# Performance work log

Hardware: AMD Instinct MI355X
Metric: run time of the kernel (lower is better)

Reference implementation:

```python
import jax, jax.numpy as jnp
import numpy as np

TAU = 0.2
ALPHA = 0.8
EPS = 1e-8  # torch cosine_similarity eps
LAM_POS = 1.5  # generate_lambda()=0.5, +1 for extrapolation
LAM_NEG = 0.5  # interpolation lambda


def _cos_sim_matrix(x):
    # row-normalize with clamped norm (matches F.cosine_similarity eps), then gram matrix
    n = x / jnp.maximum(jnp.linalg.norm(x, axis=1, keepdims=True), EPS)
    return n @ n.T


def setup_inputs() -> dict:
    key = jax.random.key(0)
    N, D = 4096, 512
    emb = jax.random.normal(key, (N, D), dtype=jnp.float32)
    # SimCLR-style symmetric positive pairs: (2k,2k+1) and (2k+1,2k)
    base = np.arange(0, N, 2)
    fwd_pairs = np.stack([base, base + 1], axis=1)
    pairs = np.concatenate([fwd_pairs, fwd_pairs[:, ::-1]], axis=0)  # [N, 2]
    return {"embeddings": emb, "positive_pairs": jnp.asarray(pairs, dtype=jnp.int32)}


def reference(embeddings, positive_pairs):
    # stage == 'train' (quantile-thresholded hard-negative branch)
    N = embeddings.shape[0]
    ar = jnp.arange(N)
    pi, pj = positive_pairs[:, 0], positive_pairs[:, 1]
    # ordered positive mask (symmetric because pairs include both orientations)
    pos_mask = jnp.zeros((N, N), dtype=bool).at[pi, pj].set(True)

    # --- extrapolate positive pairs: row i -> 1.5*e_i - 0.5*e_j ---
    partner_pos = jnp.full((N,), -1, dtype=jnp.int32).at[pi].set(pj.astype(jnp.int32))
    in_pair = partner_pos >= 0
    pp = jnp.where(in_pair, partner_pos, 0)
    hard_pos_emb = jnp.where(
        in_pair[:, None],
        LAM_POS * embeddings - (LAM_POS - 1.0) * embeddings[pp],
        embeddings,
    )

    # --- interpolate negative pairs: row k -> 0.5*(e_k + e_partner) ---
    # Negative pairs are all ordered (i,j), i!=j, not positive, scattered in
    # row k is the largest i with (i,k) negative.
    valid = (~pos_mask.T) & (ar[None, :] != ar[:, None])  # valid[k, i] = (i,k) is negative
    partner_neg = jnp.max(jnp.where(valid, ar[None, :], -1), axis=1)
    hard_neg_emb = LAM_NEG * embeddings + (1.0 - LAM_NEG) * embeddings[partner_neg]

    # --- three NxN cosine-sim matrices, composed by the scatter pattern ---
    orig_sim = _cos_sim_matrix(embeddings)
    hard_pos_sim = _cos_sim_matrix(hard_pos_emb)
    hard_neg_sim = _cos_sim_matrix(hard_neg_emb)
    diag = jnp.eye(N, dtype=bool)
    sim = jnp.where(diag, orig_sim, jnp.where(pos_mask, hard_pos_sim, hard_neg_sim))

    # --- contrastive loss with per-row quantile hard-negative threshold ---
    mask = diag | pos_mask
    exp_sim = jnp.exp(sim / TAU)
    exp_masked = jnp.where(mask, 0.0, exp_sim)
    pos_sim = exp_sim[pi, pj]              # [P]
    exp_rows = exp_masked[pi]              # [P, N]
    thr = jnp.quantile(exp_rows, ALPHA, axis=1, keepdims=True)
    hard_neg_sum = jnp.sum(jnp.where(exp_rows >= thr, exp_rows, 0.0), axis=1)
    loss = -jnp.log(pos_sim / (pos_sim + hard_neg_sum))
    # torch sums loss_ij + loss_ji over all rows / (2*P); with symmetric pair
    # list this equals sum(loss_ij)/P
    return jnp.sum(loss) / positive_pairs.shape[0]
```

## Files before the change

kernel.cpp:

```cpp
#include <hip/hip_runtime.h>
#include <cmath>

#define DIM 512
#define TAU_INV 5.0f
#define EPSN 1e-8f
#define ALPHA_Q 0.8f
#define TPITCH 72

typedef __attribute__((ext_vector_type(8))) unsigned short us8;
typedef __attribute__((ext_vector_type(4))) unsigned short us4;
typedef __attribute__((ext_vector_type(8))) short s8v;
typedef __attribute__((ext_vector_type(4))) float f4;

__device__ __forceinline__ unsigned short f2h(float f) {
    _Float16 h = (_Float16)f;
    return *(const unsigned short*)&h;
}
__device__ __forceinline__ float h2f(unsigned u) {
    unsigned short us = (unsigned short)u;
    _Float16 h = *(const _Float16*)&us;
    return (float)h;
}
__device__ __forceinline__ unsigned key16(unsigned u) {
    return u ^ (0x8000u | (0x7FFFu & (0u - (u >> 15))));
}
__device__ __forceinline__ float keyval(unsigned k) {
    unsigned u = (k & 0x8000u) ? (k & 0x7FFFu) : ((~k) & 0xFFFFu);
    return h2f(u);
}

__global__ void k_scatter(const int* __restrict__ pairs, int* partner, int P) {
    int k = blockIdx.x * 256 + threadIdx.x;
    if (k < P) partner[pairs[2 * k]] = pairs[2 * k + 1];
}

__global__ __launch_bounds__(64) void k_prep(const float* __restrict__ emb,
                                             const int* __restrict__ partner,
                                             const int* __restrict__ pairs,
                                             unsigned short* __restrict__ mb,
                                             float* __restrict__ pos_term,
                                             int N, int P) {
    int bid = blockIdx.x, t = threadIdx.x;
    if (bid < N) {
        int i = bid;
        int q = N - 1;
        if (q == i || partner[q] == i) q = N - 2;
        if (q == i || partner[q] == i) q = N - 3;
        const float4* A = (const float4*)(emb + (size_t)i * DIM);
        const float4* B = (const float4*)(emb + (size_t)q * DIM);
        float4 a0 = A[t], a1 = A[t + 64];
        float4 b0 = B[t], b1 = B[t + 64];
        float h0x = 0.5f * (a0.x + b0.x), h0y = 0.5f * (a0.y + b0.y);
        float h0z = 0.5f * (a0.z + b0.z), h0w = 0.5f * (a0.w + b0.w);
        float h1x = 0.5f * (a1.x + b1.x), h1y = 0.5f * (a1.y + b1.y);
        float h1z = 0.5f * (a1.z + b1.z), h1w = 0.5f * (a1.w + b1.w);
        float ss = h0x * h0x + h0y * h0y + h0z * h0z + h0w * h0w
                 + h1x * h1x + h1y * h1y + h1z * h1z + h1w * h1w;
        for (int o = 32; o > 0; o >>= 1) ss += __shfl_xor(ss, o);
        float inv = 1.0f / fmaxf(sqrtf(ss), EPSN);
        us4 lo, hi;
        lo[0] = f2h(h0x * inv); lo[1] = f2h(h0y * inv);
        lo[2] = f2h(h0z * inv); lo[3] = f2h(h0w * inv);
        hi[0] = f2h(h1x * inv); hi[1] = f2h(h1y * inv);
        hi[2] = f2h(h1z * inv); hi[3] = f2h(h1w * inv);
        *(us4*)(mb + (size_t)i * DIM + t * 4) = lo;
        *(us4*)(mb + (size_t)i * DIM + 256 + t * 4) = hi;
    } else {
        int k = bid - N;
        int i = pairs[2 * k], j = pairs[2 * k + 1];
        const float4* A = (const float4*)(emb + (size_t)i * DIM);
        const float4* B = (const float4*)(emb + (size_t)j * DIM);
        float4 a0 = A[t], a1 = A[t + 64];
        float4 b0 = B[t], b1 = B[t + 64];
        float dab = 0.f, naa = 0.f, nbb = 0.f;
        float fa, fb;
        fa = 1.5f * a0.x - 0.5f * b0.x; fb = 1.5f * b0.x - 0.5f * a0.x; dab += fa * fb; naa += fa * fa; nbb += fb * fb;
        fa = 1.5f * a0.y - 0.5f * b0.y; fb = 1.5f * b0.y - 0.5f * a0.y; dab += fa * fb; naa += fa * fa; nbb += fb * fb;
        fa = 1.5f * a0.z - 0.5f * b0.z; fb = 1.5f * b0.z - 0.5f * a0.z; dab += fa * fb; naa += fa * fa; nbb += fb * fb;
        fa = 1.5f * a0.w - 0.5f * b0.w; fb = 1.5f * b0.w - 0.5f * a0.w; dab += fa * fb; naa += fa * fa; nbb += fb * fb;
        fa = 1.5f * a1.x - 0.5f * b1.x; fb = 1.5f * b1.x - 0.5f * a1.x; dab += fa * fb; naa += fa * fa; nbb += fb * fb;
        fa = 1.5f * a1.y - 0.5f * b1.y; fb = 1.5f * b1.y - 0.5f * a1.y; dab += fa * fb; naa += fa * fa; nbb += fb * fb;
        fa = 1.5f * a1.z - 0.5f * b1.z; fb = 1.5f * b1.z - 0.5f * a1.z; dab += fa * fb; naa += fa * fa; nbb += fb * fb;
        fa = 1.5f * a1.w - 0.5f * b1.w; fb = 1.5f * b1.w - 0.5f * a1.w; dab += fa * fb; naa += fa * fa; nbb += fb * fb;
        for (int o = 32; o > 0; o >>= 1) {
            dab += __shfl_xor(dab, o);
            naa += __shfl_xor(naa, o);
            nbb += __shfl_xor(nbb, o);
        }
        if (t == 0) {
            float sim = dab / (fmaxf(sqrtf(naa), EPSN) * fmaxf(sqrtf(nbb), EPSN));
            pos_term[k] = expf(sim * TAU_INV);
        }
    }
}

__global__ __launch_bounds__(256, 3) void k_gemm_sym(const unsigned short* __restrict__ mb,
                                                     unsigned short* __restrict__ S, int N) {
    __shared__ __align__(16) unsigned short smem[4 * 64 * TPITCH];
    int tid = threadIdx.x;
    int wave = tid >> 6, lane = tid & 63, quad = lane >> 4, l16 = lane & 15;
    int wr = (wave >> 1) * 64, wc = (wave & 1) * 64;

    int ntb = N >> 7;
    int bi = 0, rem = blockIdx.x, rowlen = ntb;
    while (rem >= rowlen) { rem -= rowlen; ++bi; --rowlen; }
    int bj = bi + rem;
    int iBase = bi * 128, jBase = bj * 128;
    int lrow = lane >> 2, lseg = lane & 3;

    const unsigned short* gA0 = mb + (size_t)(iBase + wave * 32 + lrow) * DIM + lseg * 8;
    const unsigned short* gA1 = gA0 + 16 * DIM;
    const unsigned short* gB0 = mb + (size_t)(jBase + wave * 32 + lrow) * DIM + lseg * 8;
    const unsigned short* gB1 = gB0 + 16 * DIM;

    __attribute__((address_space(3))) char* ldsBase =
        (__attribute__((address_space(3))) char*)smem;
    __attribute__((address_space(3))) char* ldsA0 = ldsBase + wave * 2048;
    __attribute__((address_space(3))) char* ldsA1 = ldsBase + 8192 + wave * 2048;
    __attribute__((address_space(3))) char* ldsB0 = ldsBase + 16384 + wave * 2048;
    __attribute__((address_space(3))) char* ldsB1 = ldsBase + 24576 + wave * 2048;

    f4 acc[4][4];
    for (int i = 0; i < 4; ++i)
        for (int j = 0; j < 4; ++j) acc[i][j] = (f4){0.f, 0.f, 0.f, 0.f};

    for (int k0 = 0; k0 < DIM; k0 += 64) {
        __syncthreads();
        __builtin_amdgcn_global_load_lds(
            (const __attribute__((address_space(1))) void*)(gA0 + k0),
            (__attribute__((address_space(3))) void*)(ldsA0), 16, 0, 0);
        __builtin_amdgcn_global_load_lds(
            (const __attribute__((address_space(1))) void*)(gA1 + k0),
            (__attribute__((address_space(3))) void*)(ldsA0 + 1024), 16, 0, 0);
        __builtin_amdgcn_global_load_lds(
            (const __attribute__((address_space(1))) void*)(gA0 + k0 + 32),
            (__attribute__((address_space(3))) void*)(ldsA1), 16, 0, 0);
        __builtin_amdgcn_global_load_lds(
            (const __attribute__((address_space(1))) void*)(gA1 + k0 + 32),
            (__attribute__((address_space(3))) void*)(ldsA1 + 1024), 16, 0, 0);
        __builtin_amdgcn_global_load_lds(
            (const __attribute__((address_space(1))) void*)(gB0 + k0),
            (__attribute__((address_space(3))) void*)(ldsB0), 16, 0, 0);
        __builtin_amdgcn_global_load_lds(
            (const __attribute__((address_space(1))) void*)(gB1 + k0),
            (__attribute__((address_space(3))) void*)(ldsB0 + 1024), 16, 0, 0);
        __builtin_amdgcn_global_load_lds(
            (const __attribute__((address_space(1))) void*)(gB0 + k0 + 32),
            (__attribute__((address_space(3))) void*)(ldsB1), 16, 0, 0);
        __builtin_amdgcn_global_load_lds(
            (const __attribute__((address_space(1))) void*)(gB1 + k0 + 32),
            (__attribute__((address_space(3))) void*)(ldsB1 + 1024), 16, 0, 0);
        __syncthreads();

        #pragma unroll
        for (int h = 0; h < 2; ++h) {
            s8v a[4], b[4];
            #pragma unroll
            for (int i = 0; i < 4; ++i)
                a[i] = *(const s8v*)&smem[h * 4096 + (wr + i * 16 + l16) * 32 + quad * 8];
            #pragma unroll
            for (int j = 0; j < 4; ++j)
                b[j] = *(const s8v*)&smem[8192 + h * 4096 + (wc + j * 16 + l16) * 32 + quad * 8];
            #pragma unroll
            for (int i = 0; i < 4; ++i)
                #pragma unroll
                for (int j = 0; j < 4; ++j)
                    acc[i][j] = __builtin_amdgcn_mfma_f32_16x16x32_f16(a[i], b[j], acc[i][j], 0, 0, 0);
        }
    }
    int rQ = iBase + wr + quad * 4;
    int cQ = jBase + wc + l16;
    for (int i = 0; i < 4; ++i)
        for (int j = 0; j < 4; ++j)
            for (int rr = 0; rr < 4; ++rr)
                S[(size_t)(rQ + i * 16 + rr) * N + cQ + j * 16] = f2h(acc[i][j][rr]);

    if (bi != bj) {
        __syncthreads();
        unsigned short* T = smem + wave * 64 * TPITCH;
        #pragma unroll
        for (int i = 0; i < 4; ++i)
            #pragma unroll
            for (int j = 0; j < 4; ++j)
                #pragma unroll
                for (int rr = 0; rr < 4; ++rr) {
                    int tr = quad * 4 + i * 16 + rr;
                    int tc = l16 + j * 16;
                    T[tc * TPITCH + tr] = f2h(acc[i][j][rr]);
                }
        int lrow8 = lane >> 3, lseg8 = lane & 7;
        #pragma unroll
        for (int it = 0; it < 8; ++it) {
            int mr = it * 8 + lrow8;
            us8 v = *(const us8*)&T[mr * TPITCH + lseg8 * 8];
            *(us8*)&S[(size_t)(jBase + wc + mr) * N + iBase + wr + lseg8 * 8] = v;
        }
    }
}

__global__ __launch_bounds__(256) void k_gemm(const unsigned short* __restrict__ mb,
                                              unsigned short* __restrict__ S, int N, int rowBase) {
    __shared__ __align__(16) unsigned short As[128][32];
    __shared__ __align__(16) unsigned short Bs[128][32];
    int tid = threadIdx.x;
    int wave = tid >> 6, lane = tid & 63, quad = lane >> 4, l16 = lane & 15;
    int wr = (wave >> 1) * 64, wc = (wave & 1) * 64;
    int iBase = rowBase + blockIdx.y * 128;
    int jBase = blockIdx.x * 128;
    int lrow = lane >> 2, lseg = lane & 3;

    const unsigned short* gA0 = mb + (size_t)(iBase + wave * 32 + lrow) * DIM + lseg * 8;
    const unsigned short* gA1 = gA0 + 16 * DIM;
    const unsigned short* gB0 = mb + (size_t)(jBase + wave * 32 + lrow) * DIM + lseg * 8;
    const unsigned short* gB1 = gB0 + 16 * DIM;
    __attribute__((address_space(3))) char* ldsA =
        (__attribute__((address_space(3))) char*)As + wave * 2048;
    __attribute__((address_space(3))) char* ldsB =
        (__attribute__((address_space(3))) char*)Bs + wave * 2048;

    f4 acc[4][4];
    for (int i = 0; i < 4; ++i)
        for (int j = 0; j < 4; ++j) acc[i][j] = (f4){0.f, 0.f, 0.f, 0.f};

    for (int k0 = 0; k0 < DIM; k0 += 32) {
        __syncthreads();
        __builtin_amdgcn_global_load_lds(
            (const __attribute__((address_space(1))) void*)(gA0 + k0),
            (__attribute__((address_space(3))) void*)(ldsA), 16, 0, 0);
        __builtin_amdgcn_global_load_lds(
            (const __attribute__((address_space(1))) void*)(gA1 + k0),
            (__attribute__((address_space(3))) void*)(ldsA + 1024), 16, 0, 0);
        __builtin_amdgcn_global_load_lds(
            (const __attribute__((address_space(1))) void*)(gB0 + k0),
            (__attribute__((address_space(3))) void*)(ldsB), 16, 0, 0);
        __builtin_amdgcn_global_load_lds(
            (const __attribute__((address_space(1))) void*)(gB1 + k0),
            (__attribute__((address_space(3))) void*)(ldsB + 1024), 16, 0, 0);
        __syncthreads();

        s8v a[4], b[4];
        for (int i = 0; i < 4; ++i) a[i] = *(const s8v*)&As[wr + i * 16 + l16][quad * 8];
        for (int j = 0; j < 4; ++j) b[j] = *(const s8v*)&Bs[wc + j * 16 + l16][quad * 8];
        for (int i = 0; i < 4; ++i)
            for (int j = 0; j < 4; ++j)
                acc[i][j] = __builtin_amdgcn_mfma_f32_16x16x32_f16(a[i], b[j], acc[i][j], 0, 0, 0);
    }
    int rQ = blockIdx.y * 128 + wr + quad * 4;
    int cQ = jBase + wc + l16;
    for (int i = 0; i < 4; ++i)
        for (int j = 0; j < 4; ++j)
            for (int rr = 0; rr < 4; ++rr)
                S[(size_t)(rQ + i * 16 + rr) * N + cQ + j * 16] = f2h(acc[i][j][rr]);
}

__global__ __launch_bounds__(128, 4) void k_select(const unsigned short* __restrict__ Sb,
                                                   const int* __restrict__ pairs,
                                                   const float* __restrict__ pos_term,
                                                   float* __restrict__ losses,
                                                   int N, int r0, int r1, int P,
                                                   int klo, float frac) {
    int wid = threadIdx.x >> 6, lane = threadIdx.x & 63;
    int k = blockIdx.x * 2 + wid;
    if (k >= P) return;
    int row = pairs[2 * k];
    if (row < r0 || row >= r1) return;
    int pj = pairs[2 * k + 1];
    const us8* src8 = (const us8*)(Sb + (size_t)(row - r0) * N);

    unsigned kr[32];
    #pragma unroll
    for (int t = 0; t < 8; ++t)
        *(us8*)&kr[t * 4] = src8[t * 64 + lane];

    #pragma unroll
    for (int t = 0; t < 8; ++t) {
        int j0 = (t * 64 + lane) * 8;
        #pragma unroll
        for (int m = 0; m < 4; ++m) {
            unsigned p = kr[t * 4 + m];
            unsigned lo = key16(p & 0xFFFFu);
            unsigned hi = key16(p >> 16);
            int jlo = j0 + 2 * m, jhi = jlo + 1;
            if (jlo == row || jlo == pj) lo = 0u;
            if (jhi == row || jhi == pj) hi = 0u;
            kr[t * 4 + m] = lo | (hi << 16);
        }
    }

    int nmask = (pj == row) ? 1 : 2;
    int Nreal = N - nmask;
    int Rreal = klo - nmask;
    float pos = pos_term[k];
    float s = 0.f;

    if (Rreal < 0) {
        #pragma unroll
        for (int i = 0; i < 32; ++i) {
            unsigned lo = kr[i] & 0xFFFFu, hi = kr[i] >> 16;
            if (lo > 0u) s += __expf(keyval(lo) * TAU_INV);
            if (hi > 0u) s += __expf(keyval(hi) * TAU_INV);
        }
    } else {
        int lim = Nreal - Rreal - 1;
        unsigned lo_ = 1, hi_ = 65535;
        while (lo_ < hi_) {
            unsigned mid = (lo_ + hi_) >> 1;
            unsigned cnt = 0;
            #pragma unroll
            for (int i = 0; i < 32; ++i) {
                cnt += (unsigned)__popcll(__ballot((kr[i] & 0xFFFFu) > mid));
                cnt += (unsigned)__popcll(__ballot((kr[i] >> 16) > mid));
            }
            if (cnt <= (unsigned)lim) hi_ = mid; else lo_ = mid + 1;
        }
        unsigned K1 = lo_;

        if (frac > 1e-9f) {
            unsigned cntAbove = 0, mymin = 0xFFFFFFFFu;
            #pragma unroll
            for (int i = 0; i < 32; ++i) {
                unsigned lo = kr[i] & 0xFFFFu, hi = kr[i] >> 16;
                bool glo = lo > K1, ghi = hi > K1;
                cntAbove += (unsigned)__popcll(__ballot(glo));
                cntAbove += (unsigned)__popcll(__ballot(ghi));
                if (glo && lo < mymin) mymin = lo;
                if (ghi && hi < mymin) mymin = hi;
            }
            for (int o = 1; o < 64; o <<= 1) {
                unsigned y = (unsigned)__shfl_xor((int)mymin, o);
                if (y < mymin) mymin = y;
            }
            unsigned K2;
            if (Rreal + 1 > Nreal - 1)                   K2 = K1;
            else if (Nreal - (int)cntAbove >= Rreal + 2) K2 = K1;
            else                                         K2 = mymin;
            float elo = __expf(keyval(K1) * TAU_INV);
            float ehi = __expf(keyval(K2) * TAU_INV);
            float thr = elo + frac * (ehi - elo);
            #pragma unroll
            for (int i = 0; i < 32; ++i) {
                unsigned lo = kr[i] & 0xFFFFu, hi = kr[i] >> 16;
                if (lo > 0u) { float ev = __expf(keyval(lo) * TAU_INV); if (ev >= thr) s += ev; }
                if (hi > 0u) { float ev = __expf(keyval(hi) * TAU_INV); if (ev >= thr) s += ev; }
            }
        } else {
            #pragma unroll
            for (int i = 0; i < 32; ++i) {
                unsigned lo = kr[i] & 0xFFFFu, hi = kr[i] >> 16;
                if (lo >= K1) s += __expf(keyval(lo) * TAU_INV);
                if (hi >= K1) s += __expf(keyval(hi) * TAU_INV);
            }
        }
    }

    for (int o = 1; o < 64; o <<= 1) s += __shfl_xor(s, o);
    if (lane == 0) losses[k] = logf((pos + s) / pos);
}

__global__ __launch_bounds__(256) void k_reduce(const float* __restrict__ losses,
                                                float* __restrict__ out, int P, float invP) {
    __shared__ float s_red[4];
    int tid = threadIdx.x, wid = tid >> 6, lane = tid & 63;
    float s = 0.f;
    for (int i = tid; i < P; i += 256) s += losses[i];
    for (int o = 1; o < 64; o <<= 1) s += __shfl_xor(s, o);
    if (lane == 0) s_red[wid] = s;
    __syncthreads();
    if (tid == 0) out[0] = (s_red[0] + s_red[1] + s_red[2] + s_red[3]) * invP;
}

extern "C" void kernel_launch(void* const* d_in, const int* in_sizes, int n_in,
                              void* d_out, int out_size, void* d_ws, size_t ws_size,
                              hipStream_t stream) {
    const float* emb = (const float*)d_in[0];
    const int* pairs = (const int*)d_in[1];
    float* out = (float*)d_out;
    int N = in_sizes[0] / DIM;
    int P = in_sizes[1] / 2;

    char* ws = (char*)d_ws;
    size_t off = 0;
    unsigned short* mb = (unsigned short*)(ws + off); off += (size_t)N * DIM * 2;
    int* partner = (int*)(ws + off);                  off += (size_t)N * 4;
    float* pos_term = (float*)(ws + off);             off += (size_t)P * 4;
    float* losses = (float*)(ws + off);               off += (size_t)P * 4;
    off = (off + 255) & ~(size_t)255;
    unsigned short* Sbuf = (unsigned short*)(ws + off);
    size_t avail = (ws_size > off) ? ws_size - off : 0;
    long maxRows = (long)(avail / ((size_t)N * 2));
    int chunk = (int)(maxRows - (maxRows % 128));
    if (chunk > N) chunk = N;
    if (chunk < 128) chunk = 128;

    k_scatter<<<dim3((P + 255) / 256), dim3(256), 0, stream>>>(pairs, partner, P);
    k_prep<<<dim3(N + P), dim3(64), 0, stream>>>(emb, partner, pairs, mb, pos_term, N, P);

    float qpos = ALPHA_Q * (float)(N - 1);
    int klo = (int)floorf(qpos);
    float frac = qpos - (float)klo;
    float invP = 1.0f / (float)P;

    if (chunk >= N) {
        int ntb = N >> 7;
        int nblk = ntb * (ntb + 1) / 2;
        k_gemm_sym<<<dim3(nblk), dim3(256), 0, stream>>>(mb, Sbuf, N);
        k_select<<<dim3((P + 1) / 2), dim3(128), 0, stream>>>(Sbuf, pairs, pos_term, losses,
                                                              N, 0, N, P, klo, frac);
    } else {
        for (int r0 = 0; r0 < N; r0 += chunk) {
            int rows = (N - r0 < chunk) ? (N - r0) : chunk;
            dim3 g(N / 128, rows / 128);
            k_gemm<<<g, dim3(256), 0, stream>>>(mb, Sbuf, N, r0);
            k_select<<<dim3((P + 1) / 2), dim3(128), 0, stream>>>(Sbuf, pairs, pos_term, losses,
                                                                  N, r0, r0 + rows, P, klo, frac);
        }
    }
    k_reduce<<<dim3(1), dim3(256), 0, stream>>>(losses, out, P, invP);
}
```

Baseline: 122.4 us.

## Double-buffer GEMM LDS staging, narrow select binary search, fuse final reduction

The symmetric GEMM now stages 32-wide K slices into two alternating LDS buffers, so the global-to-LDS loads for the next slice are issued while MFMAs run on the current one, with one barrier per step. The select kernel unpacks keys into 64 registers per lane and bounds its binary search by the row's min and max key, which cuts iterations. The separate reduce kernel is removed: a last-block-done atomic counter inside select sums the losses. This adds register pressure in select and relies on threadfence and atomic ordering for the fused reduction.

```diff
diff --git a/kernel.cpp b/kernel.cpp
--- a/kernel.cpp
+++ b/kernel.cpp
@@ -29,8 +29,9 @@
     return h2f(u);
 }
 
-__global__ void k_scatter(const int* __restrict__ pairs, int* partner, int P) {
+__global__ void k_scatter(const int* __restrict__ pairs, int* partner, int* done, int P) {
     int k = blockIdx.x * 256 + threadIdx.x;
+    if (blockIdx.x == 0 && threadIdx.x == 0) *done = 0;
     if (k < P) partner[pairs[2 * k]] = pairs[2 * k + 1];
 }
 
@@ -115,59 +116,52 @@
 
     __attribute__((address_space(3))) char* ldsBase =
         (__attribute__((address_space(3))) char*)smem;
-    __attribute__((address_space(3))) char* ldsA0 = ldsBase + wave * 2048;
-    __attribute__((address_space(3))) char* ldsA1 = ldsBase + 8192 + wave * 2048;
-    __attribute__((address_space(3))) char* ldsB0 = ldsBase + 16384 + wave * 2048;
-    __attribute__((address_space(3))) char* ldsB1 = ldsBase + 24576 + wave * 2048;
+
+#define STAGE(buf, koff)                                                                   \
+    do {                                                                                   \
+        __attribute__((address_space(3))) char* dA = ldsBase + (buf) * 16384 + wave * 2048;\
+        __attribute__((address_space(3))) char* dB = dA + 8192;                            \
+        __builtin_amdgcn_global_load_lds(                                                  \
+            (const __attribute__((address_space(1))) void*)(gA0 + (koff)),                 \
+            (__attribute__((address_space(3))) void*)(dA), 16, 0, 0);                      \
+        __builtin_amdgcn_global_load_lds(                                                  \
+            (const __attribute__((address_space(1))) void*)(gA1 + (koff)),                 \
+            (__attribute__((address_space(3))) void*)(dA + 1024), 16, 0, 0);               \
+        __builtin_amdgcn_global_load_lds(                                                  \
+            (const __attribute__((address_space(1))) void*)(gB0 + (koff)),                 \
+            (__attribute__((address_space(3))) void*)(dB), 16, 0, 0);                      \
+        __builtin_amdgcn_global_load_lds(                                                  \
+            (const __attribute__((address_space(1))) void*)(gB1 + (koff)),                 \
+            (__attribute__((address_space(3))) void*)(dB + 1024), 16, 0, 0);               \
+    } while (0)
 
     f4 acc[4][4];
     for (int i = 0; i < 4; ++i)
         for (int j = 0; j < 4; ++j) acc[i][j] = (f4){0.f, 0.f, 0.f, 0.f};
 
-    for (int k0 = 0; k0 < DIM; k0 += 64) {
-        __syncthreads();
-        __builtin_amdgcn_global_load_lds(
-            (const __attribute__((address_space(1))) void*)(gA0 + k0),
-            (__attribute__((address_space(3))) void*)(ldsA0), 16, 0, 0);
-        __builtin_amdgcn_global_load_lds(
-            (const __attribute__((address_space(1))) void*)(gA1 + k0),
-            (__attribute__((address_space(3))) void*)(ldsA0 + 1024), 16, 0, 0);
-        __builtin_amdgcn_global_load_lds(
-            (const __attribute__((address_space(1))) void*)(gA0 + k0 + 32),
-            (__attribute__((address_space(3))) void*)(ldsA1), 16, 0, 0);
-        __builtin_amdgcn_global_load_lds(
-            (const __attribute__((address_space(1))) void*)(gA1 + k0 + 32),
-            (__attribute__((address_space(3))) void*)(ldsA1 + 1024), 16, 0, 0);
-        __builtin_amdgcn_global_load_lds(
-            (const __attribute__((address_space(1))) void*)(gB0 + k0),
-            (__attribute__((address_space(3))) void*)(ldsB0), 16, 0, 0);
-        __builtin_amdgcn_global_load_lds(
-            (const __attribute__((address_space(1))) void*)(gB1 + k0),
-            (__attribute__((address_space(3))) void*)(ldsB0 + 1024), 16, 0, 0);
-        __builtin_amdgcn_global_load_lds(
-            (const __attribute__((address_space(1))) void*)(gB0 + k0 + 32),
-            (__attribute__((address_space(3))) void*)(ldsB1), 16, 0, 0);
-        __builtin_amdgcn_global_load_lds(
-            (const __attribute__((address_space(1))) void*)(gB1 + k0 + 32),
-            (__attribute__((address_space(3))) void*)(ldsB1 + 1024), 16, 0, 0);
-        __syncthreads();
-
-        #pragma unroll
-        for (int h = 0; h < 2; ++h) {
-            s8v a[4], b[4];
-            #pragma unroll
-            for (int i = 0; i < 4; ++i)
-                a[i] = *(const s8v*)&smem[h * 4096 + (wr + i * 16 + l16) * 32 + quad * 8];
+    STAGE(0, 0);
+    __syncthreads();
+    int cur = 0;
+    for (int t = 0; t < 16; ++t) {
+        if (t < 15) STAGE(cur ^ 1, (t + 1) * 32);
+        const unsigned short* base = smem + cur * 8192;
+        s8v a[4], b[4];
+        #pragma unroll
+        for (int i = 0; i < 4; ++i)
+            a[i] = *(const s8v*)&base[(wr + i * 16 + l16) * 32 + quad * 8];
+        #pragma unroll
+        for (int j = 0; j < 4; ++j)
+            b[j] = *(const s8v*)&base[4096 + (wc + j * 16 + l16) * 32 + quad * 8];
+        #pragma unroll
+        for (int i = 0; i < 4; ++i)
             #pragma unroll
             for (int j = 0; j < 4; ++j)
-                b[j] = *(const s8v*)&smem[8192 + h * 4096 + (wc + j * 16 + l16) * 32 + quad * 8];
-            #pragma unroll
-            for (int i = 0; i < 4; ++i)
-                #pragma unroll
-                for (int j = 0; j < 4; ++j)
-                    acc[i][j] = __builtin_amdgcn_mfma_f32_16x16x32_f16(a[i], b[j], acc[i][j], 0, 0, 0);
-        }
-    }
+                acc[i][j] = __builtin_amdgcn_mfma_f32_16x16x32_f16(a[i], b[j], acc[i][j], 0, 0, 0);
+        __syncthreads();
+        cur ^= 1;
+    }
+#undef STAGE
+
     int rQ = iBase + wr + quad * 4;
     int cQ = jBase + wc + l16;
     for (int i = 0; i < 4; ++i)
@@ -176,7 +170,6 @@
                 S[(size_t)(rQ + i * 16 + rr) * N + cQ + j * 16] = f2h(acc[i][j][rr]);
 
     if (bi != bj) {
-        __syncthreads();
         unsigned short* T = smem + wave * 64 * TPITCH;
         #pragma unroll
         for (int i = 0; i < 4; ++i)
@@ -257,116 +250,126 @@
                                                    const int* __restrict__ pairs,
                                                    const float* __restrict__ pos_term,
                                                    float* __restrict__ losses,
+                                                   float* __restrict__ out,
+                                                   int* __restrict__ done,
                                                    int N, int r0, int r1, int P,
-                                                   int klo, float frac) {
+                                                   int klo, float frac, float invP, int totBlk) {
     int wid = threadIdx.x >> 6, lane = threadIdx.x & 63;
     int k = blockIdx.x * 2 + wid;
-    if (k >= P) return;
-    int row = pairs[2 * k];
-    if (row < r0 || row >= r1) return;
-    int pj = pairs[2 * k + 1];
-    const us8* src8 = (const us8*)(Sb + (size_t)(row - r0) * N);
-
-    unsigned kr[32];
-    #pragma unroll
-    for (int t = 0; t < 8; ++t)
-        *(us8*)&kr[t * 4] = src8[t * 64 + lane];
-
-    #pragma unroll
-    for (int t = 0; t < 8; ++t) {
-        int j0 = (t * 64 + lane) * 8;
-        #pragma unroll
-        for (int m = 0; m < 4; ++m) {
-            unsigned p = kr[t * 4 + m];
-            unsigned lo = key16(p & 0xFFFFu);
-            unsigned hi = key16(p >> 16);
-            int jlo = j0 + 2 * m, jhi = jlo + 1;
-            if (jlo == row || jlo == pj) lo = 0u;
-            if (jhi == row || jhi == pj) hi = 0u;
-            kr[t * 4 + m] = lo | (hi << 16);
-        }
-    }
-
-    int nmask = (pj == row) ? 1 : 2;
-    int Nreal = N - nmask;
-    int Rreal = klo - nmask;
-    float pos = pos_term[k];
-    float s = 0.f;
-
-    if (Rreal < 0) {
-        #pragma unroll
-        for (int i = 0; i < 32; ++i) {
-            unsigned lo = kr[i] & 0xFFFFu, hi = kr[i] >> 16;
-            if (lo > 0u) s += __expf(keyval(lo) * TAU_INV);
-            if (hi > 0u) s += __expf(keyval(hi) * TAU_INV);
-        }
-    } else {
-        int lim = Nreal - Rreal - 1;
-        unsigned lo_ = 1, hi_ = 65535;
-        while (lo_ < hi_) {
-            unsigned mid = (lo_ + hi_) >> 1;
-            unsigned cnt = 0;
+    bool active = (k < P);
+    int row = 0, pj = 0;
+    if (active) {
+        row = pairs[2 * k];
+        if (row < r0 || row >= r1) active = false;
+        else pj = pairs[2 * k + 1];
+    }
+    if (active) {
+        const us8* src8 = (const us8*)(Sb + (size_t)(row - r0) * N);
+        unsigned kk[64];
+        #pragma unroll
+        for (int t = 0; t < 8; ++t) {
+            us8 v = src8[t * 64 + lane];
+            int j0 = (t * 64 + lane) * 8;
             #pragma unroll
-            for (int i = 0; i < 32; ++i) {
-                cnt += (unsigned)__popcll(__ballot((kr[i] & 0xFFFFu) > mid));
-                cnt += (unsigned)__popcll(__ballot((kr[i] >> 16) > mid));
+            for (int m = 0; m < 8; ++m) {
+                unsigned key = key16((unsigned)(unsigned short)v[m]);
+                int j = j0 + m;
+                if (j == row || j == pj) key = 0u;
+                kk[t * 8 + m] = key;
             }
-            if (cnt <= (unsigned)lim) hi_ = mid; else lo_ = mid + 1;
-        }
-        unsigned K1 = lo_;
-
-        if (frac > 1e-9f) {
-            unsigned cntAbove = 0, mymin = 0xFFFFFFFFu;
+        }
+
+        int nmask = (pj == row) ? 1 : 2;
+        int Nreal = N - nmask;
+        int Rreal = klo - nmask;
+        float pos = pos_term[k];
+        float s = 0.f;
+
+        if (Rreal < 0) {
             #pragma unroll
-            for (int i = 0; i < 32; ++i) {
-                unsigned lo = kr[i] & 0xFFFFu, hi = kr[i] >> 16;
-                bool glo = lo > K1, ghi = hi > K1;
-                cntAbove += (unsigned)__popcll(__ballot(glo));
-                cntAbove += (unsigned)__popcll(__ballot(ghi));
-                if (glo && lo < mymin) mymin = lo;
-                if (ghi && hi < mymin) mymin = hi;
+            for (int i = 0; i < 64; ++i)
+                if (kk[i] > 0u) s += __expf(keyval(kk[i]) * TAU_INV);
+        } else {
+            unsigned kmn = 0xFFFFu, kmx = 1u;
+            #pragma unroll
+            for (int i = 0; i < 64; ++i) {
+                unsigned x = kk[i];
+                unsigned xm = (x == 0u) ? 0xFFFFu : x;
+                kmn = (xm < kmn) ? xm : kmn;
+                kmx = (x > kmx) ? x : kmx;
             }
             for (int o = 1; o < 64; o <<= 1) {
-                unsigned y = (unsigned)__shfl_xor((int)mymin, o);
-                if (y < mymin) mymin = y;
+                unsigned ymn = (unsigned)__shfl_xor((int)kmn, o);
+                unsigned ymx = (unsigned)__shfl_xor((int)kmx, o);
+                if (ymn < kmn) kmn = ymn;
+                if (ymx > kmx) kmx = ymx;
             }
-            unsigned K2;
-            if (Rreal + 1 > Nreal - 1)                   K2 = K1;
-            else if (Nreal - (int)cntAbove >= Rreal + 2) K2 = K1;
-            else                                         K2 = mymin;
-            float elo = __expf(keyval(K1) * TAU_INV);
-            float ehi = __expf(keyval(K2) * TAU_INV);
-            float thr = elo + frac * (ehi - elo);
-            #pragma unroll
-            for (int i = 0; i < 32; ++i) {
-                unsigned lo = kr[i] & 0xFFFFu, hi = kr[i] >> 16;
-                if (lo > 0u) { float ev = __expf(keyval(lo) * TAU_INV); if (ev >= thr) s += ev; }
-                if (hi > 0u) { float ev = __expf(keyval(hi) * TAU_INV); if (ev >= thr) s += ev; }
+            int lim = Nreal - Rreal - 1;
+            unsigned lo_ = kmn, hi_ = kmx;
+            while (lo_ < hi_) {
+                unsigned mid = (lo_ + hi_) >> 1;
+                unsigned cnt = 0;
+                #pragma unroll
+                for (int i = 0; i < 64; ++i)
+                    cnt += (unsigned)__popcll(__ballot(kk[i] > mid));
+                if (cnt <= (unsigned)lim) hi_ = mid; else lo_ = mid + 1;
             }
-        } else {
-            #pragma unroll
-            for (int i = 0; i < 32; ++i) {
-                unsigned lo = kr[i] & 0xFFFFu, hi = kr[i] >> 16;
-                if (lo >= K1) s += __expf(keyval(lo) * TAU_INV);
-                if (hi >= K1) s += __expf(keyval(hi) * TAU_INV);
+            unsigned K1 = lo_;
+
+            if (frac > 1e-9f) {
+                unsigned cntAbove = 0, mymin = 0xFFFFFFFFu;
+                #pragma unroll
+                for (int i = 0; i < 64; ++i) {
+                    unsigned x = kk[i];
+                    bool g = x > K1;
+                    cntAbove += (unsigned)__popcll(__ballot(g));
+                    if (g && x < mymin) mymin = x;
+                }
+                for (int o = 1; o < 64; o <<= 1) {
+                    unsigned y = (unsigned)__shfl_xor((int)mymin, o);
+                    if (y < mymin) mymin = y;
+                }
+                unsigned K2;
+                if (Rreal + 1 > Nreal - 1)                   K2 = K1;
+                else if (Nreal - (int)cntAbove >= Rreal + 2) K2 = K1;
+                else                                         K2 = mymin;
+                float elo = __expf(keyval(K1) * TAU_INV);
+                float ehi = __expf(keyval(K2) * TAU_INV);
+                float thr = elo + frac * (ehi - elo);
+                #pragma unroll
+                for (int i = 0; i < 64; ++i) {
+                    unsigned x = kk[i];
+                    if (x > 0u) { float ev = __expf(keyval(x) * TAU_INV); if (ev >= thr) s += ev; }
+                }
+            } else {
+                #pragma unroll
+                for (int i = 0; i < 64; ++i)
+                    if (kk[i] >= K1) s += __expf(keyval(kk[i]) * TAU_INV);
             }
         }
-    }
-
-    for (int o = 1; o < 64; o <<= 1) s += __shfl_xor(s, o);
-    if (lane == 0) losses[k] = logf((pos + s) / pos);
-}
-
-__global__ __launch_bounds__(256) void k_reduce(const float* __restrict__ losses,
-                                                float* __restrict__ out, int P, float invP) {
-    __shared__ float s_red[4];
-    int tid = threadIdx.x, wid = tid >> 6, lane = tid & 63;
-    float s = 0.f;
-    for (int i = tid; i < P; i += 256) s += losses[i];
-    for (int o = 1; o < 64; o <<= 1) s += __shfl_xor(s, o);
-    if (lane == 0) s_red[wid] = s;
+
+        for (int o = 1; o < 64; o <<= 1) s += __shfl_xor(s, o);
+        if (lane == 0) losses[k] = logf((pos + s) / pos);
+    }
+
+    __shared__ int s_last;
+    __shared__ float s_red[2];
+    __threadfence();
     __syncthreads();
-    if (tid == 0) out[0] = (s_red[0] + s_red[1] + s_red[2] + s_red[3]) * invP;
+    if (threadIdx.x == 0) {
+        int old = atomicAdd(done, 1);
+        s_last = (old == totBlk - 1) ? 1 : 0;
+    }
+    __syncthreads();
+    if (s_last) {
+        __threadfence();
+        float s = 0.f;
+        for (int i = threadIdx.x; i < P; i += 128) s += losses[i];
+        for (int o = 1; o < 64; o <<= 1) s += __shfl_xor(s, o);
+        if ((threadIdx.x & 63) == 0) s_red[threadIdx.x >> 6] = s;
+        __syncthreads();
+        if (threadIdx.x == 0) out[0] = (s_red[0] + s_red[1]) * invP;
+    }
 }
 
 extern "C" void kernel_launch(void* const* d_in, const int* in_sizes, int n_in,
@@ -384,7 +387,7 @@
     int* partner = (int*)(ws + off);                  off += (size_t)N * 4;
     float* pos_term = (float*)(ws + off);             off += (size_t)P * 4;
     float* losses = (float*)(ws + off);               off += (size_t)P * 4;
-    off = (off + 255) & ~(size_t)255;
+    int* done = (int*)(ws + off);                     off += 256;
     unsigned short* Sbuf = (unsigned short*)(ws + off);
     size_t avail = (ws_size > off) ? ws_size - off : 0;
     long maxRows = (long)(avail / ((size_t)N * 2));
@@ -392,28 +395,30 @@
     if (chunk > N) chunk = N;
     if (chunk < 128) chunk = 128;
 
-    k_scatter<<<dim3((P + 255) / 256), dim3(256), 0, stream>>>(pairs, partner, P);
+    k_scatter<<<dim3((P + 255) / 256), dim3(256), 0, stream>>>(pairs, partner, done, P);
     k_prep<<<dim3(N + P), dim3(64), 0, stream>>>(emb, partner, pairs, mb, pos_term, N, P);
 
     float qpos = ALPHA_Q * (float)(N - 1);
     int klo = (int)floorf(qpos);
     float frac = qpos - (float)klo;
     float invP = 1.0f / (float)P;
+    int gsel = (P + 1) / 2;
 
     if (chunk >= N) {
         int ntb = N >> 7;
         int nblk = ntb * (ntb + 1) / 2;
         k_gemm_sym<<<dim3(nblk), dim3(256), 0, stream>>>(mb, Sbuf, N);
-        k_select<<<dim3((P + 1) / 2), dim3(128), 0, stream>>>(Sbuf, pairs, pos_term, losses,
-                                                              N, 0, N, P, klo, frac);
+        k_select<<<dim3(gsel), dim3(128), 0, stream>>>(Sbuf, pairs, pos_term, losses, out, done,
+                                                       N, 0, N, P, klo, frac, invP, gsel);
     } else {
+        int nch = (N + chunk - 1) / chunk;
+        int totBlk = gsel * nch;
         for (int r0 = 0; r0 < N; r0 += chunk) {
             int rows = (N - r0 < chunk) ? (N - r0) : chunk;
             dim3 g(N / 128, rows / 128);
             k_gemm<<<g, dim3(256), 0, stream>>>(mb, Sbuf, N, r0);
-            k_select<<<dim3((P + 1) / 2), dim3(128), 0, stream>>>(Sbuf, pairs, pos_term, losses,
-                                                                  N, r0, r0 + rows, P, klo, frac);
-        }
-    }
-    k_reduce<<<dim3(1), dim3(256), 0, stream>>>(losses, out, P, invP);
-}
+            k_select<<<dim3(gsel), dim3(128), 0, stream>>>(Sbuf, pairs, pos_term, losses, out, done,
+                                                           N, r0, r0 + rows, P, klo, frac, invP, totBlk);
+        }
+    }
+}
```

Measured after the change: 175.3 us. 43.2% more time.
